# Kernel tuning notes

Hardware: AMD Instinct MI355X
Metric: run time of the kernel (lower is better)

Reference implementation:

```python
import jax, jax.numpy as jnp
import numpy as np

TOP_K = 2


def setup_inputs() -> dict:
    key = jax.random.key(0)
    k0, k1, k2, k3 = jax.random.split(key, 4)
    T, H, E, I = 512, 2048, 16, 1024  # tokens, hidden, experts, intermediate
    return {
        "hidden_states": jax.random.normal(k0, (T, H), jnp.float32),
        "router_weight": jax.random.normal(k1, (E, H), jnp.float32) * 0.02,
        "w13": jax.random.normal(k2, (E, H, 2 * I), jnp.float32) * 0.02,  # fused gate+up
        "w2": jax.random.normal(k3, (E, I, H), jnp.float32) * 0.02,        # down proj
    }


def reference(hidden_states, router_weight, w13, w2):
    x = hidden_states                                   # [T, H]
    E = router_weight.shape[0]
    # Router: linear (no bias) -> softmax -> top-k -> renormalize
    logits = x @ router_weight.T                        # [T, E]
    probs = jax.nn.softmax(logits, axis=-1)
    vals, idx = jax.lax.top_k(probs, TOP_K)             # [T, K]
    vals = vals / jnp.sum(vals, axis=-1, keepdims=True)
    # Dense combine weights [T, E]: zero except the top-k experts per token
    cw = jnp.sum(jax.nn.one_hot(idx, E, dtype=x.dtype) * vals[..., None], axis=1)
    # Scan over experts; each expert runs a SwiGLU MLP over all tokens,
    # scaled by its (mostly-zero) combine weight. Keeps peak memory at [T, I].
    def body(acc, params):
        w13_e, w2_e, cw_e = params                      # [H,2I], [I,H], [T]
        g, u = jnp.split(x @ w13_e, 2, axis=-1)         # [T, I] each
        acc = acc + cw_e[:, None] * ((jax.nn.silu(g) * u) @ w2_e)
        return acc, None
    out, _ = jax.lax.scan(body, jnp.zeros_like(x), (w13, w2, cw.T))
    return out
```

## Files before the change

kernel.cpp:

```cpp
#include <hip/hip_runtime.h>

#define T_TOK 512
#define HID   2048
#define NEXP  16
#define IDIM  1024
#define KC    64
#define WSTRIDE 2048

typedef __attribute__((ext_vector_type(8)))  short bf16x8;
typedef __attribute__((ext_vector_type(16))) float f32x16;
typedef __attribute__((ext_vector_type(4)))  float float4v;

__device__ __forceinline__ unsigned short f2bf(float f) {
    union { float f; unsigned u; } v; v.f = f;
    return (unsigned short)((v.u + 0x7FFFu + ((v.u >> 16) & 1u)) >> 16);
}

__device__ __forceinline__ bf16x8 pack8(const float* s) {
    bf16x8 r;
#pragma unroll
    for (int i = 0; i < 8; ++i) r[i] = (short)f2bf(s[i]);
    return r;
}

__global__ __launch_bounds__(256) void router_kernel(
    const float* __restrict__ x, const float* __restrict__ rw,
    int* __restrict__ cnt, int* __restrict__ tok,
    int* __restrict__ rowid, float* __restrict__ wt,
    unsigned short* __restrict__ xb)
{
    int t = blockIdx.x;
    int tid = threadIdx.x;
    const float* xr = x + (size_t)t * HID;

    {
        int c = tid * 8;
        float4v a = *(const float4v*)(xr + c);
        float4v b = *(const float4v*)(xr + c + 4);
        float tmp[8];
#pragma unroll
        for (int i = 0; i < 4; ++i) { tmp[i] = a[i]; tmp[4 + i] = b[i]; }
        *(bf16x8*)(xb + (size_t)t * HID + c) = pack8(tmp);
    }

    float acc[NEXP];
#pragma unroll
    for (int e = 0; e < NEXP; ++e) acc[e] = 0.f;

    for (int k = tid; k < HID; k += 256) {
        float xv = xr[k];
#pragma unroll
        for (int e = 0; e < NEXP; ++e) acc[e] += xv * rw[e * HID + k];
    }

    __shared__ float red[4][NEXP];
    int lane = tid & 63, wv = tid >> 6;
#pragma unroll
    for (int e = 0; e < NEXP; ++e) {
        float v = acc[e];
#pragma unroll
        for (int off = 32; off > 0; off >>= 1) v += __shfl_down(v, off);
        if (lane == 0) red[wv][e] = v;
    }
    __syncthreads();

    if (tid == 0) {
        float l[NEXP];
        float mx = -1e30f;
#pragma unroll
        for (int e = 0; e < NEXP; ++e) {
            l[e] = red[0][e] + red[1][e] + red[2][e] + red[3][e];
            mx = fmaxf(mx, l[e]);
        }
        float s = 0.f;
#pragma unroll
        for (int e = 0; e < NEXP; ++e) { l[e] = __expf(l[e] - mx); s += l[e]; }
        float inv_s = 1.f / s;
        int i0 = 0; float v0 = -1.f;
        int i1 = 0; float v1 = -2.f;
#pragma unroll
        for (int e = 0; e < NEXP; ++e) {
            float p = l[e] * inv_s;
            if (p > v0)      { v1 = v0; i1 = i0; v0 = p; i0 = e; }
            else if (p > v1) { v1 = p; i1 = e; }
        }
        float inv = 1.f / (v0 + v1);
        int p0 = atomicAdd(&cnt[i0], 1);
        tok[i0 * T_TOK + p0] = t; rowid[i0 * T_TOK + p0] = 2 * t;     wt[i0 * T_TOK + p0] = v0 * inv;
        int p1 = atomicAdd(&cnt[i1], 1);
        tok[i1 * T_TOK + p1] = t; rowid[i1 * T_TOK + p1] = 2 * t + 1; wt[i1 * T_TOK + p1] = v1 * inv;
    }
}

#define LOADW(r, kk_) { _Pragma("unroll") for (int j = 0; j < 8; ++j) \
    r[j] = wsrc[(size_t)((kk_) + kq * 8 + j) * WSTRIDE]; }

#define STOREW(r, bufi) { \
    *(bf16x8*)((char*)Ws[bufi] + ((wcol * 128 + kq * 16) ^ ((wcol & 7) << 4))) = pack8(r); }

#define LOADX(r, kk_) { \
    r[0] = *(const bf16x8*)(xsrc + (kk_)); \
    r[1] = *(const bf16x8*)(xsrc + (kk_) + 8); }

#define STOREX(r, bufi) { \
    *(bf16x8*)((char*)Xs[bufi] + ((xrow * 128 + xq * 32)      ^ xswz)) = r[0]; \
    *(bf16x8*)((char*)Xs[bufi] + ((xrow * 128 + xq * 32 + 16) ^ xswz)) = r[1]; }

__global__ __launch_bounds__(512, 4) void gemm1_kernel(
    const unsigned short* __restrict__ xb, const float* __restrict__ w13,
    const int* __restrict__ cnt, const int* __restrict__ tok,
    const int* __restrict__ rowid, const float* __restrict__ wt,
    unsigned short* __restrict__ h)
{
    int bid = blockIdx.x;
    int e   = bid >> 5;
    int c0h = (bid & 31) * 32;
    int n = cnt[e];
    int tid = threadIdx.x;

    __shared__ __align__(16) short Xs[2][128 * KC];
    __shared__ __align__(16) short Ws[2][64 * KC];
    __shared__ float Ex[4][16][64];
    __shared__ int   tks[128];
    __shared__ int   rws[128];
    __shared__ float wts[128];

    const float* wbase = w13 + (size_t)e * HID * (2 * IDIM);

    int wcol = tid & 63, kq = tid >> 6;
    const float* wsrc = wbase + ((wcol < 32) ? (c0h + wcol)
                                             : (IDIM + c0h + (wcol - 32)));
    int xrow = tid >> 2, xq = tid & 3;
    int xswz = (xrow & 7) << 4;

    int wave = tid >> 6, lane = tid & 63;
    int wm = wave & 3, wn = wave >> 2;
    int lrow = lane & 31, lhalf = lane >> 5;
    int swz = (lrow & 7) << 4;

#define G1_MFMA(bufi) { if (wm * 32 < nt) { _Pragma("unroll") \
    for (int s = 0; s < 4; ++s) { \
        int kb = s * 32 + lhalf * 16; \
        bf16x8 a = *(const bf16x8*)((char*)Xs[bufi] + (((wm * 32 + lrow) * 128 + kb) ^ swz)); \
        bf16x8 b = *(const bf16x8*)((char*)Ws[bufi] + (((wn * 32 + lrow) * 128 + kb) ^ swz)); \
        acc = __builtin_amdgcn_mfma_f32_32x32x16_bf16(a, b, acc, 0, 0, 0); \
    } } }

    for (int t0 = 0; t0 < n; t0 += 128) {
        int nt = min(128, n - t0);
        __syncthreads();
        if (tid < 128) {
            int idx = t0 + min(tid, nt - 1);
            tks[tid] = tok[e * T_TOK + idx];
            rws[tid] = rowid[e * T_TOK + idx];
            wts[tid] = wt[e * T_TOK + idx];
        }
        __syncthreads();

        const unsigned short* xsrc = xb + (size_t)tks[xrow] * HID + xq * 16;

        f32x16 acc = (f32x16)0.f;
        float  rWa[8], rWb[8];
        bf16x8 rXa[2], rXb[2];

        LOADW(rWa, 0);  LOADX(rXa, 0);
        LOADW(rWb, KC); LOADX(rXb, KC);
        STOREW(rWa, 0); STOREX(rXa, 0);
        __syncthreads();

        for (int p = 0; p < HID / KC; p += 2) {
            int kf0 = (p + 2) * KC, kf1 = (p + 3) * KC;
            if (kf0 < HID) { LOADW(rWa, kf0); LOADX(rXa, kf0); }
            G1_MFMA(0);
            STOREW(rWb, 1); STOREX(rXb, 1);
            __syncthreads();
            if (kf1 < HID) { LOADW(rWb, kf1); LOADX(rXb, kf1); }
            G1_MFMA(1);
            if (kf0 < HID) { STOREW(rWa, 0); STOREX(rXa, 0); }
            __syncthreads();
        }

        if (wn == 1) {
#pragma unroll
            for (int q = 0; q < 16; ++q) Ex[wm][q][lane] = acc[q];
        }
        __syncthreads();
        if (wn == 0) {
#pragma unroll
            for (int q = 0; q < 16; ++q) {
                int r = wm * 32 + (q & 3) + 8 * (q >> 2) + 4 * lhalf;
                if (r < nt) {
                    float g = acc[q];
                    float u = Ex[wm][q][lane];
                    float sg = g / (1.f + __expf(-g));
                    h[(size_t)rws[r] * IDIM + c0h + lrow] = f2bf(wts[r] * sg * u);
                }
            }
        }
    }
}

__global__ __launch_bounds__(512, 4) void gemm2_kernel(
    const unsigned short* __restrict__ h, const float* __restrict__ w2,
    const int* __restrict__ cnt, const int* __restrict__ tok,
    const int* __restrict__ rowid,
    float* __restrict__ out)
{
    int bid = blockIdx.x;
    int e  = bid >> 5;
    int c0 = (bid & 31) * 64;
    int n = cnt[e];
    int tid = threadIdx.x;

    __shared__ __align__(16) short Xs[2][128 * KC];
    __shared__ __align__(16) short Ws[2][64 * KC];
    __shared__ int   tks[128];
    __shared__ int   rws[128];

    const float* wbase = w2 + (size_t)e * IDIM * HID;

    int wcol = tid & 63, kq = tid >> 6;
    const float* wsrc = wbase + c0 + wcol;
    int xrow = tid >> 2, xq = tid & 3;
    int xswz = (xrow & 7) << 4;

    int wave = tid >> 6, lane = tid & 63;
    int wm = wave & 3, wn = wave >> 2;
    int lrow = lane & 31, lhalf = lane >> 5;
    int swz = (lrow & 7) << 4;

#define G2_MFMA(bufi) { if (wm * 32 < nt) { _Pragma("unroll") \
    for (int s = 0; s < 4; ++s) { \
        int kb = s * 32 + lhalf * 16; \
        bf16x8 a = *(const bf16x8*)((char*)Xs[bufi] + (((wm * 32 + lrow) * 128 + kb) ^ swz)); \
        bf16x8 b = *(const bf16x8*)((char*)Ws[bufi] + (((wn * 32 + lrow) * 128 + kb) ^ swz)); \
        acc = __builtin_amdgcn_mfma_f32_32x32x16_bf16(a, b, acc, 0, 0, 0); \
    } } }

    for (int t0 = 0; t0 < n; t0 += 128) {
        int nt = min(128, n - t0);
        __syncthreads();
        if (tid < 128) {
            int idx = t0 + min(tid, nt - 1);
            tks[tid] = tok[e * T_TOK + idx];
            rws[tid] = rowid[e * T_TOK + idx];
        }
        __syncthreads();

        const unsigned short* xsrc = h + (size_t)rws[xrow] * IDIM + xq * 16;

        f32x16 acc = (f32x16)0.f;
        float  rWa[8], rWb[8];
        bf16x8 rXa[2], rXb[2];

        LOADW(rWa, 0);  LOADX(rXa, 0);
        LOADW(rWb, KC); LOADX(rXb, KC);
        STOREW(rWa, 0); STOREX(rXa, 0);
        __syncthreads();

        for (int p = 0; p < IDIM / KC; p += 2) {
            int kf0 = (p + 2) * KC, kf1 = (p + 3) * KC;
            if (kf0 < IDIM) { LOADW(rWa, kf0); LOADX(rXa, kf0); }
            G2_MFMA(0);
            STOREW(rWb, 1); STOREX(rXb, 1);
            __syncthreads();
            if (kf1 < IDIM) { LOADW(rWb, kf1); LOADX(rXb, kf1); }
            G2_MFMA(1);
            if (kf0 < IDIM) { STOREW(rWa, 0); STOREX(rXa, 0); }
            __syncthreads();
        }

#pragma unroll
        for (int q = 0; q < 16; ++q) {
            int r = wm * 32 + (q & 3) + 8 * (q >> 2) + 4 * lhalf;
            if (r < nt)
                atomicAdd(&out[(size_t)tks[r] * HID + c0 + wn * 32 + lrow], acc[q]);
        }
    }
}

extern "C" void kernel_launch(void* const* d_in, const int* in_sizes, int n_in,
                              void* d_out, int out_size, void* d_ws, size_t ws_size,
                              hipStream_t stream) {
    const float* x   = (const float*)d_in[0];
    const float* rw  = (const float*)d_in[1];
    const float* w13 = (const float*)d_in[2];
    const float* w2  = (const float*)d_in[3];
    float* out = (float*)d_out;

    int* cnt   = (int*)d_ws;
    int* tok   = cnt + 64;
    int* rowid = tok + NEXP * T_TOK;
    float* wt  = (float*)(rowid + NEXP * T_TOK);
    unsigned short* h  = (unsigned short*)((char*)d_ws + 131072);
    unsigned short* xb = (unsigned short*)((char*)d_ws + 131072 + 2097152);

    hipMemsetAsync(out, 0, (size_t)T_TOK * HID * sizeof(float), stream);
    hipMemsetAsync(cnt, 0, 64 * sizeof(int), stream);

    router_kernel<<<T_TOK, 256, 0, stream>>>(x, rw, cnt, tok, rowid, wt, xb);
    gemm1_kernel<<<512, 512, 0, stream>>>(xb, w13, cnt, tok, rowid, wt, h);
    gemm2_kernel<<<512, 512, 0, stream>>>(h, w2, cnt, tok, rowid, out);
}
```

Baseline: 134.6 us.

## Split-K both expert GEMMs with wider tiles, atomic accumulation and separate SiLU pass

Both GEMMs are restructured as split-K. Each block now covers a 256-column by 512-row (gemm1) or 256-row (gemm2) K slice and uses 1024 threads with two accumulators per wave. Gemm1 atomically accumulates fp32 gate/up partials into a new workspace buffer, and a new silu_kernel applies SiLU, the gate×up product and the routing weight, storing bf16 h. This targets the long serial K loops and low per-block parallelism, and makes each block's weight loads wider. The cost is an extra memset and kernel launch, fp32 atomic traffic on the gate/up buffer, and loss of the double-buffered LDS pipeline.

```diff
diff --git a/kernel.cpp b/kernel.cpp
--- a/kernel.cpp
+++ b/kernel.cpp
@@ -5,7 +5,7 @@
 #define NEXP  16
 #define IDIM  1024
 #define KC    64
-#define WSTRIDE 2048
+#define W2I   2048
 
 typedef __attribute__((ext_vector_type(8)))  short bf16x8;
 typedef __attribute__((ext_vector_type(16))) float f32x16;
@@ -26,7 +26,7 @@
 __global__ __launch_bounds__(256) void router_kernel(
     const float* __restrict__ x, const float* __restrict__ rw,
     int* __restrict__ cnt, int* __restrict__ tok,
-    int* __restrict__ rowid, float* __restrict__ wt,
+    int* __restrict__ rowid, float* __restrict__ wtrow,
     unsigned short* __restrict__ xb)
 {
     int t = blockIdx.x;
@@ -86,65 +86,42 @@
         }
         float inv = 1.f / (v0 + v1);
         int p0 = atomicAdd(&cnt[i0], 1);
-        tok[i0 * T_TOK + p0] = t; rowid[i0 * T_TOK + p0] = 2 * t;     wt[i0 * T_TOK + p0] = v0 * inv;
+        tok[i0 * T_TOK + p0] = t; rowid[i0 * T_TOK + p0] = 2 * t;
         int p1 = atomicAdd(&cnt[i1], 1);
-        tok[i1 * T_TOK + p1] = t; rowid[i1 * T_TOK + p1] = 2 * t + 1; wt[i1 * T_TOK + p1] = v1 * inv;
-    }
-}
-
-#define LOADW(r, kk_) { _Pragma("unroll") for (int j = 0; j < 8; ++j) \
-    r[j] = wsrc[(size_t)((kk_) + kq * 8 + j) * WSTRIDE]; }
-
-#define STOREW(r, bufi) { \
-    *(bf16x8*)((char*)Ws[bufi] + ((wcol * 128 + kq * 16) ^ ((wcol & 7) << 4))) = pack8(r); }
-
-#define LOADX(r, kk_) { \
-    r[0] = *(const bf16x8*)(xsrc + (kk_)); \
-    r[1] = *(const bf16x8*)(xsrc + (kk_) + 8); }
-
-#define STOREX(r, bufi) { \
-    *(bf16x8*)((char*)Xs[bufi] + ((xrow * 128 + xq * 32)      ^ xswz)) = r[0]; \
-    *(bf16x8*)((char*)Xs[bufi] + ((xrow * 128 + xq * 32 + 16) ^ xswz)) = r[1]; }
-
-__global__ __launch_bounds__(512, 4) void gemm1_kernel(
+        tok[i1 * T_TOK + p1] = t; rowid[i1 * T_TOK + p1] = 2 * t + 1;
+        wtrow[2 * t]     = v0 * inv;
+        wtrow[2 * t + 1] = v1 * inv;
+    }
+}
+
+__global__ __launch_bounds__(1024, 4) void gemm1_kernel(
     const unsigned short* __restrict__ xb, const float* __restrict__ w13,
     const int* __restrict__ cnt, const int* __restrict__ tok,
-    const int* __restrict__ rowid, const float* __restrict__ wt,
-    unsigned short* __restrict__ h)
+    const int* __restrict__ rowid,
+    float* __restrict__ gu)
 {
     int bid = blockIdx.x;
     int e   = bid >> 5;
-    int c0h = (bid & 31) * 32;
+    int c0  = ((bid >> 2) & 7) * 256;
+    int kc0 = (bid & 3) * 512;
     int n = cnt[e];
     int tid = threadIdx.x;
 
-    __shared__ __align__(16) short Xs[2][128 * KC];
-    __shared__ __align__(16) short Ws[2][64 * KC];
-    __shared__ float Ex[4][16][64];
-    __shared__ int   tks[128];
-    __shared__ int   rws[128];
-    __shared__ float wts[128];
-
-    const float* wbase = w13 + (size_t)e * HID * (2 * IDIM);
-
-    int wcol = tid & 63, kq = tid >> 6;
-    const float* wsrc = wbase + ((wcol < 32) ? (c0h + wcol)
-                                             : (IDIM + c0h + (wcol - 32)));
-    int xrow = tid >> 2, xq = tid & 3;
+    __shared__ __align__(16) short Xs[128 * KC];
+    __shared__ __align__(16) short Ws[256 * KC];
+    __shared__ int tks[128];
+    __shared__ int rws[128];
+
+    int wcol = tid & 255, kq = (tid >> 8) & 3;
+    const float* wsrc = w13 + (size_t)e * HID * W2I + c0 + wcol;
+    int wswz = (wcol & 7) << 4;
+    int xrow = tid >> 3, xq = tid & 7;
     int xswz = (xrow & 7) << 4;
 
     int wave = tid >> 6, lane = tid & 63;
     int wm = wave & 3, wn = wave >> 2;
     int lrow = lane & 31, lhalf = lane >> 5;
     int swz = (lrow & 7) << 4;
-
-#define G1_MFMA(bufi) { if (wm * 32 < nt) { _Pragma("unroll") \
-    for (int s = 0; s < 4; ++s) { \
-        int kb = s * 32 + lhalf * 16; \
-        bf16x8 a = *(const bf16x8*)((char*)Xs[bufi] + (((wm * 32 + lrow) * 128 + kb) ^ swz)); \
-        bf16x8 b = *(const bf16x8*)((char*)Ws[bufi] + (((wn * 32 + lrow) * 128 + kb) ^ swz)); \
-        acc = __builtin_amdgcn_mfma_f32_32x32x16_bf16(a, b, acc, 0, 0, 0); \
-    } } }
 
     for (int t0 = 0; t0 < n; t0 += 128) {
         int nt = min(128, n - t0);
@@ -153,89 +130,106 @@
             int idx = t0 + min(tid, nt - 1);
             tks[tid] = tok[e * T_TOK + idx];
             rws[tid] = rowid[e * T_TOK + idx];
-            wts[tid] = wt[e * T_TOK + idx];
         }
         __syncthreads();
 
-        const unsigned short* xsrc = xb + (size_t)tks[xrow] * HID + xq * 16;
-
-        f32x16 acc = (f32x16)0.f;
-        float  rWa[8], rWb[8];
-        bf16x8 rXa[2], rXb[2];
-
-        LOADW(rWa, 0);  LOADX(rXa, 0);
-        LOADW(rWb, KC); LOADX(rXb, KC);
-        STOREW(rWa, 0); STOREX(rXa, 0);
-        __syncthreads();
-
-        for (int p = 0; p < HID / KC; p += 2) {
-            int kf0 = (p + 2) * KC, kf1 = (p + 3) * KC;
-            if (kf0 < HID) { LOADW(rWa, kf0); LOADX(rXa, kf0); }
-            G1_MFMA(0);
-            STOREW(rWb, 1); STOREX(rXb, 1);
+        const unsigned short* xsrc = xb + (size_t)tks[xrow] * HID + kc0 + xq * 8;
+
+        f32x16 acc0 = (f32x16)0.f, acc1 = (f32x16)0.f;
+        float  rW[16];
+        bf16x8 rX;
+
+#pragma unroll
+        for (int j = 0; j < 16; ++j)
+            rW[j] = wsrc[(size_t)(kc0 + kq * 16 + j) * W2I];
+        rX = *(const bf16x8*)(xsrc);
+
+        for (int p = 0; p < 8; ++p) {
+            *(bf16x8*)((char*)Ws + ((wcol * 128 + kq * 32)      ^ wswz)) = pack8(&rW[0]);
+            *(bf16x8*)((char*)Ws + ((wcol * 128 + kq * 32 + 16) ^ wswz)) = pack8(&rW[8]);
+            *(bf16x8*)((char*)Xs + ((xrow * 128 + xq * 16) ^ xswz)) = rX;
+            if (p < 7) {
+                int k0n = kc0 + (p + 1) * KC;
+#pragma unroll
+                for (int j = 0; j < 16; ++j)
+                    rW[j] = wsrc[(size_t)(k0n + kq * 16 + j) * W2I];
+                rX = *(const bf16x8*)(xsrc + (p + 1) * KC);
+            }
             __syncthreads();
-            if (kf1 < HID) { LOADW(rWb, kf1); LOADX(rXb, kf1); }
-            G1_MFMA(1);
-            if (kf0 < HID) { STOREW(rWa, 0); STOREX(rXa, 0); }
+            if (wm * 32 < nt) {
+#pragma unroll
+                for (int s = 0; s < 4; ++s) {
+                    int kb = s * 32 + lhalf * 16;
+                    bf16x8 a  = *(const bf16x8*)((char*)Xs + (((wm * 32 + lrow) * 128 + kb) ^ swz));
+                    bf16x8 b0 = *(const bf16x8*)((char*)Ws + (((wn * 64 + lrow) * 128 + kb) ^ swz));
+                    acc0 = __builtin_amdgcn_mfma_f32_32x32x16_bf16(a, b0, acc0, 0, 0, 0);
+                    bf16x8 b1 = *(const bf16x8*)((char*)Ws + (((wn * 64 + 32 + lrow) * 128 + kb) ^ swz));
+                    acc1 = __builtin_amdgcn_mfma_f32_32x32x16_bf16(a, b1, acc1, 0, 0, 0);
+                }
+            }
             __syncthreads();
         }
 
-        if (wn == 1) {
-#pragma unroll
-            for (int q = 0; q < 16; ++q) Ex[wm][q][lane] = acc[q];
-        }
-        __syncthreads();
-        if (wn == 0) {
-#pragma unroll
-            for (int q = 0; q < 16; ++q) {
-                int r = wm * 32 + (q & 3) + 8 * (q >> 2) + 4 * lhalf;
-                if (r < nt) {
-                    float g = acc[q];
-                    float u = Ex[wm][q][lane];
-                    float sg = g / (1.f + __expf(-g));
-                    h[(size_t)rws[r] * IDIM + c0h + lrow] = f2bf(wts[r] * sg * u);
-                }
-            }
-        }
-    }
-}
-
-__global__ __launch_bounds__(512, 4) void gemm2_kernel(
+#pragma unroll
+        for (int q = 0; q < 16; ++q) {
+            int r = wm * 32 + (q & 3) + 8 * (q >> 2) + 4 * lhalf;
+            if (r < nt) {
+                size_t rowb = (size_t)rws[r] * W2I + c0 + wn * 64 + lrow;
+                atomicAdd(&gu[rowb], acc0[q]);
+                atomicAdd(&gu[rowb + 32], acc1[q]);
+            }
+        }
+    }
+}
+
+__global__ __launch_bounds__(256) void silu_kernel(
+    const float* __restrict__ gu, const float* __restrict__ wtrow,
+    unsigned short* __restrict__ h)
+{
+    int r = blockIdx.x;
+    int c = threadIdx.x * 4;
+    float w = wtrow[r];
+    float4v g = *(const float4v*)(gu + (size_t)r * W2I + c);
+    float4v u = *(const float4v*)(gu + (size_t)r * W2I + IDIM + c);
+    unsigned o01, o23;
+    float s0 = g[0] / (1.f + __expf(-g[0])) * u[0] * w;
+    float s1 = g[1] / (1.f + __expf(-g[1])) * u[1] * w;
+    float s2 = g[2] / (1.f + __expf(-g[2])) * u[2] * w;
+    float s3 = g[3] / (1.f + __expf(-g[3])) * u[3] * w;
+    o01 = (unsigned)f2bf(s0) | ((unsigned)f2bf(s1) << 16);
+    o23 = (unsigned)f2bf(s2) | ((unsigned)f2bf(s3) << 16);
+    unsigned* dst = (unsigned*)(h + (size_t)r * IDIM + c);
+    dst[0] = o01; dst[1] = o23;
+}
+
+__global__ __launch_bounds__(1024, 4) void gemm2_kernel(
     const unsigned short* __restrict__ h, const float* __restrict__ w2,
     const int* __restrict__ cnt, const int* __restrict__ tok,
     const int* __restrict__ rowid,
     float* __restrict__ out)
 {
     int bid = blockIdx.x;
-    int e  = bid >> 5;
-    int c0 = (bid & 31) * 64;
+    int e   = bid >> 5;
+    int c0  = ((bid >> 2) & 7) * 256;
+    int kc0 = (bid & 3) * 256;
     int n = cnt[e];
     int tid = threadIdx.x;
 
-    __shared__ __align__(16) short Xs[2][128 * KC];
-    __shared__ __align__(16) short Ws[2][64 * KC];
-    __shared__ int   tks[128];
-    __shared__ int   rws[128];
-
-    const float* wbase = w2 + (size_t)e * IDIM * HID;
-
-    int wcol = tid & 63, kq = tid >> 6;
-    const float* wsrc = wbase + c0 + wcol;
-    int xrow = tid >> 2, xq = tid & 3;
+    __shared__ __align__(16) short Xs[128 * KC];
+    __shared__ __align__(16) short Ws[256 * KC];
+    __shared__ int tks[128];
+    __shared__ int rws[128];
+
+    int wcol = tid & 255, kq = (tid >> 8) & 3;
+    const float* wsrc = w2 + (size_t)e * IDIM * HID + c0 + wcol;
+    int wswz = (wcol & 7) << 4;
+    int xrow = tid >> 3, xq = tid & 7;
     int xswz = (xrow & 7) << 4;
 
     int wave = tid >> 6, lane = tid & 63;
     int wm = wave & 3, wn = wave >> 2;
     int lrow = lane & 31, lhalf = lane >> 5;
     int swz = (lrow & 7) << 4;
-
-#define G2_MFMA(bufi) { if (wm * 32 < nt) { _Pragma("unroll") \
-    for (int s = 0; s < 4; ++s) { \
-        int kb = s * 32 + lhalf * 16; \
-        bf16x8 a = *(const bf16x8*)((char*)Xs[bufi] + (((wm * 32 + lrow) * 128 + kb) ^ swz)); \
-        bf16x8 b = *(const bf16x8*)((char*)Ws[bufi] + (((wn * 32 + lrow) * 128 + kb) ^ swz)); \
-        acc = __builtin_amdgcn_mfma_f32_32x32x16_bf16(a, b, acc, 0, 0, 0); \
-    } } }
 
     for (int t0 = 0; t0 < n; t0 += 128) {
         int nt = min(128, n - t0);
@@ -247,34 +241,51 @@
         }
         __syncthreads();
 
-        const unsigned short* xsrc = h + (size_t)rws[xrow] * IDIM + xq * 16;
-
-        f32x16 acc = (f32x16)0.f;
-        float  rWa[8], rWb[8];
-        bf16x8 rXa[2], rXb[2];
-
-        LOADW(rWa, 0);  LOADX(rXa, 0);
-        LOADW(rWb, KC); LOADX(rXb, KC);
-        STOREW(rWa, 0); STOREX(rXa, 0);
-        __syncthreads();
-
-        for (int p = 0; p < IDIM / KC; p += 2) {
-            int kf0 = (p + 2) * KC, kf1 = (p + 3) * KC;
-            if (kf0 < IDIM) { LOADW(rWa, kf0); LOADX(rXa, kf0); }
-            G2_MFMA(0);
-            STOREW(rWb, 1); STOREX(rXb, 1);
+        const unsigned short* xsrc = h + (size_t)rws[xrow] * IDIM + kc0 + xq * 8;
+
+        f32x16 acc0 = (f32x16)0.f, acc1 = (f32x16)0.f;
+        float  rW[16];
+        bf16x8 rX;
+
+#pragma unroll
+        for (int j = 0; j < 16; ++j)
+            rW[j] = wsrc[(size_t)(kc0 + kq * 16 + j) * W2I];
+        rX = *(const bf16x8*)(xsrc);
+
+        for (int p = 0; p < 4; ++p) {
+            *(bf16x8*)((char*)Ws + ((wcol * 128 + kq * 32)      ^ wswz)) = pack8(&rW[0]);
+            *(bf16x8*)((char*)Ws + ((wcol * 128 + kq * 32 + 16) ^ wswz)) = pack8(&rW[8]);
+            *(bf16x8*)((char*)Xs + ((xrow * 128 + xq * 16) ^ xswz)) = rX;
+            if (p < 3) {
+                int k0n = kc0 + (p + 1) * KC;
+#pragma unroll
+                for (int j = 0; j < 16; ++j)
+                    rW[j] = wsrc[(size_t)(k0n + kq * 16 + j) * W2I];
+                rX = *(const bf16x8*)(xsrc + (p + 1) * KC);
+            }
             __syncthreads();
-            if (kf1 < IDIM) { LOADW(rWb, kf1); LOADX(rXb, kf1); }
-            G2_MFMA(1);
-            if (kf0 < IDIM) { STOREW(rWa, 0); STOREX(rXa, 0); }
+            if (wm * 32 < nt) {
+#pragma unroll
+                for (int s = 0; s < 4; ++s) {
+                    int kb = s * 32 + lhalf * 16;
+                    bf16x8 a  = *(const bf16x8*)((char*)Xs + (((wm * 32 + lrow) * 128 + kb) ^ swz));
+                    bf16x8 b0 = *(const bf16x8*)((char*)Ws + (((wn * 64 + lrow) * 128 + kb) ^ swz));
+                    acc0 = __builtin_amdgcn_mfma_f32_32x32x16_bf16(a, b0, acc0, 0, 0, 0);
+                    bf16x8 b1 = *(const bf16x8*)((char*)Ws + (((wn * 64 + 32 + lrow) * 128 + kb) ^ swz));
+                    acc1 = __builtin_amdgcn_mfma_f32_32x32x16_bf16(a, b1, acc1, 0, 0, 0);
+                }
+            }
             __syncthreads();
         }
 
 #pragma unroll
         for (int q = 0; q < 16; ++q) {
             int r = wm * 32 + (q & 3) + 8 * (q >> 2) + 4 * lhalf;
-            if (r < nt)
-                atomicAdd(&out[(size_t)tks[r] * HID + c0 + wn * 32 + lrow], acc[q]);
+            if (r < nt) {
+                size_t ob = (size_t)tks[r] * HID + c0 + wn * 64 + lrow;
+                atomicAdd(&out[ob], acc0[q]);
+                atomicAdd(&out[ob + 32], acc1[q]);
+            }
         }
     }
 }
@@ -288,17 +299,21 @@
     const float* w2  = (const float*)d_in[3];
     float* out = (float*)d_out;
 
-    int* cnt   = (int*)d_ws;
-    int* tok   = cnt + 64;
-    int* rowid = tok + NEXP * T_TOK;
-    float* wt  = (float*)(rowid + NEXP * T_TOK);
-    unsigned short* h  = (unsigned short*)((char*)d_ws + 131072);
-    unsigned short* xb = (unsigned short*)((char*)d_ws + 131072 + 2097152);
+    char* ws = (char*)d_ws;
+    int*   cnt   = (int*)ws;
+    int*   tok   = (int*)(ws + 1024);
+    int*   rowid = (int*)(ws + 1024 + 32768);
+    float* wtrow = (float*)(ws + 1024 + 65536);
+    unsigned short* h  = (unsigned short*)(ws + 131072);
+    unsigned short* xb = (unsigned short*)(ws + 131072 + 2097152);
+    float* gu = (float*)(ws + 131072 + 2 * 2097152);
 
     hipMemsetAsync(out, 0, (size_t)T_TOK * HID * sizeof(float), stream);
-    hipMemsetAsync(cnt, 0, 64 * sizeof(int), stream);
-
-    router_kernel<<<T_TOK, 256, 0, stream>>>(x, rw, cnt, tok, rowid, wt, xb);
-    gemm1_kernel<<<512, 512, 0, stream>>>(xb, w13, cnt, tok, rowid, wt, h);
-    gemm2_kernel<<<512, 512, 0, stream>>>(h, w2, cnt, tok, rowid, out);
-}
+    hipMemsetAsync(cnt, 0, 1024, stream);
+    hipMemsetAsync(gu, 0, (size_t)1024 * W2I * sizeof(float), stream);
+
+    router_kernel<<<T_TOK, 256, 0, stream>>>(x, rw, cnt, tok, rowid, wtrow, xb);
+    gemm1_kernel<<<512, 1024, 0, stream>>>(xb, w13, cnt, tok, rowid, gu);
+    silu_kernel<<<1024, 256, 0, stream>>>(gu, wtrow, h);
+    gemm2_kernel<<<512, 1024, 0, stream>>>(h, w2, cnt, tok, rowid, out);
+}
```

After: 164.3 us. +22.1%, slower.

## Stage large token chunks in LDS and stream fp32 weights directly into MFMA registers

Applied to the files above, without the earlier changes.

Both expert GEMM kernels are restructured. Each block now stages a 128x512 bf16 token slice in a 128KB shared buffer, and each wave loads its weight B-fragments straight from global memory into registers, packing them to bf16 without a shared-memory round trip. Each wave computes two 32x32 output tiles, reusing one B fragment across two MFMAs, and the grid is halved to 256 blocks with larger column tiles. This removes the weight LDS staging and its per-step barriers, at the cost of lower occupancy, uncoalesced strided weight loads per lane, and fewer blocks to fill the GPU.

```diff
diff --git a/kernel.cpp b/kernel.cpp
--- a/kernel.cpp
+++ b/kernel.cpp
@@ -4,8 +4,6 @@
 #define HID   2048
 #define NEXP  16
 #define IDIM  1024
-#define KC    64
-#define WSTRIDE 2048
 
 typedef __attribute__((ext_vector_type(8)))  short bf16x8;
 typedef __attribute__((ext_vector_type(16))) float f32x16;
@@ -92,59 +90,46 @@
     }
 }
 
-#define LOADW(r, kk_) { _Pragma("unroll") for (int j = 0; j < 8; ++j) \
-    r[j] = wsrc[(size_t)((kk_) + kq * 8 + j) * WSTRIDE]; }
-
-#define STOREW(r, bufi) { \
-    *(bf16x8*)((char*)Ws[bufi] + ((wcol * 128 + kq * 16) ^ ((wcol & 7) << 4))) = pack8(r); }
-
-#define LOADX(r, kk_) { \
-    r[0] = *(const bf16x8*)(xsrc + (kk_)); \
-    r[1] = *(const bf16x8*)(xsrc + (kk_) + 8); }
-
-#define STOREX(r, bufi) { \
-    *(bf16x8*)((char*)Xs[bufi] + ((xrow * 128 + xq * 32)      ^ xswz)) = r[0]; \
-    *(bf16x8*)((char*)Xs[bufi] + ((xrow * 128 + xq * 32 + 16) ^ xswz)) = r[1]; }
-
-__global__ __launch_bounds__(512, 4) void gemm1_kernel(
+#define STAGE_X(SRCROW) { \
+    const bf16x8* src16 = (const bf16x8*)((SRCROW) + kc0 + xseg * 128); \
+    _Pragma("unroll") \
+    for (int q = 0; q < 16; ++q) { \
+        bf16x8 v = src16[q]; \
+        *(bf16x8*)((char*)Xs + ((xrow * 1024 + xseg * 256 + q * 16) ^ xswz)) = v; \
+    } }
+
+#define LOADB(buf, p_) { _Pragma("unroll") \
+    for (int j = 0; j < 8; ++j) \
+        buf[j] = wsrc[(size_t)(kc0 + (p_) * 16 + j) * 2048]; }
+
+__global__ __launch_bounds__(512, 2) void gemm1_kernel(
     const unsigned short* __restrict__ xb, const float* __restrict__ w13,
     const int* __restrict__ cnt, const int* __restrict__ tok,
     const int* __restrict__ rowid, const float* __restrict__ wt,
     unsigned short* __restrict__ h)
 {
     int bid = blockIdx.x;
-    int e   = bid >> 5;
-    int c0h = (bid & 31) * 32;
+    int e    = bid >> 4;
+    int tile = bid & 15;
     int n = cnt[e];
     int tid = threadIdx.x;
 
-    __shared__ __align__(16) short Xs[2][128 * KC];
-    __shared__ __align__(16) short Ws[2][64 * KC];
-    __shared__ float Ex[4][16][64];
+    __shared__ __align__(16) short Xs[65536];
     __shared__ int   tks[128];
     __shared__ int   rws[128];
     __shared__ float wts[128];
 
-    const float* wbase = w13 + (size_t)e * HID * (2 * IDIM);
-
-    int wcol = tid & 63, kq = tid >> 6;
-    const float* wsrc = wbase + ((wcol < 32) ? (c0h + wcol)
-                                             : (IDIM + c0h + (wcol - 32)));
-    int xrow = tid >> 2, xq = tid & 3;
+    int xrow = tid >> 2, xseg = tid & 3;
     int xswz = (xrow & 7) << 4;
 
     int wave = tid >> 6, lane = tid & 63;
-    int wm = wave & 3, wn = wave >> 2;
-    int lrow = lane & 31, lhalf = lane >> 5;
+    int wm = wave & 1, wn = wave >> 1;
+    int lrow = lane & 31, hi = lane >> 5;
     int swz = (lrow & 7) << 4;
 
-#define G1_MFMA(bufi) { if (wm * 32 < nt) { _Pragma("unroll") \
-    for (int s = 0; s < 4; ++s) { \
-        int kb = s * 32 + lhalf * 16; \
-        bf16x8 a = *(const bf16x8*)((char*)Xs[bufi] + (((wm * 32 + lrow) * 128 + kb) ^ swz)); \
-        bf16x8 b = *(const bf16x8*)((char*)Ws[bufi] + (((wn * 32 + lrow) * 128 + kb) ^ swz)); \
-        acc = __builtin_amdgcn_mfma_f32_32x32x16_bf16(a, b, acc, 0, 0, 0); \
-    } } }
+    int col = (wn < 2) ? (tile * 64 + wn * 32 + lrow)
+                       : (IDIM + tile * 64 + (wn - 2) * 32 + lrow);
+    const float* wsrc = w13 + (size_t)e * HID * 2048 + col + (size_t)hi * 8 * 2048;
 
     for (int t0 = 0; t0 < n; t0 += 128) {
         int nt = min(128, n - t0);
@@ -157,85 +142,105 @@
         }
         __syncthreads();
 
-        const unsigned short* xsrc = xb + (size_t)tks[xrow] * HID + xq * 16;
-
-        f32x16 acc = (f32x16)0.f;
-        float  rWa[8], rWb[8];
-        bf16x8 rXa[2], rXb[2];
-
-        LOADW(rWa, 0);  LOADX(rXa, 0);
-        LOADW(rWb, KC); LOADX(rXb, KC);
-        STOREW(rWa, 0); STOREX(rXa, 0);
-        __syncthreads();
-
-        for (int p = 0; p < HID / KC; p += 2) {
-            int kf0 = (p + 2) * KC, kf1 = (p + 3) * KC;
-            if (kf0 < HID) { LOADW(rWa, kf0); LOADX(rXa, kf0); }
-            G1_MFMA(0);
-            STOREW(rWb, 1); STOREX(rXb, 1);
+        const unsigned short* xrowp = xb + (size_t)tks[xrow] * HID;
+        bool g0 = (wm * 64) < nt, g1 = (wm * 64 + 32) < nt;
+        int r0 = (wm * 64 + lrow) * 1024;
+        int r1 = r0 + 32 * 1024;
+
+        f32x16 acc0 = (f32x16)0.f, acc1 = (f32x16)0.f;
+
+        for (int c = 0; c < 4; ++c) {
+            int kc0 = c * 512;
+            STAGE_X(xrowp);
             __syncthreads();
-            if (kf1 < HID) { LOADW(rWb, kf1); LOADX(rXb, kf1); }
-            G1_MFMA(1);
-            if (kf0 < HID) { STOREW(rWa, 0); STOREX(rXa, 0); }
+
+            float b0[8], b1[8];
+            LOADB(b0, 0); LOADB(b1, 1);
+#pragma unroll 4
+            for (int p = 0; p < 32; p += 2) {
+                bf16x8 bfr = pack8(b0);
+                if (p + 2 < 32) LOADB(b0, p + 2);
+                {
+                    int kb = p * 32 + hi * 16;
+                    bf16x8 a0 = *(const bf16x8*)((char*)Xs + ((r0 + kb) ^ swz));
+                    bf16x8 a1 = *(const bf16x8*)((char*)Xs + ((r1 + kb) ^ swz));
+                    if (g0) acc0 = __builtin_amdgcn_mfma_f32_32x32x16_bf16(a0, bfr, acc0, 0, 0, 0);
+                    if (g1) acc1 = __builtin_amdgcn_mfma_f32_32x32x16_bf16(a1, bfr, acc1, 0, 0, 0);
+                }
+                bf16x8 bfr1 = pack8(b1);
+                if (p + 3 < 32) LOADB(b1, p + 3);
+                {
+                    int kb = (p + 1) * 32 + hi * 16;
+                    bf16x8 a0 = *(const bf16x8*)((char*)Xs + ((r0 + kb) ^ swz));
+                    bf16x8 a1 = *(const bf16x8*)((char*)Xs + ((r1 + kb) ^ swz));
+                    if (g0) acc0 = __builtin_amdgcn_mfma_f32_32x32x16_bf16(a0, bfr1, acc0, 0, 0, 0);
+                    if (g1) acc1 = __builtin_amdgcn_mfma_f32_32x32x16_bf16(a1, bfr1, acc1, 0, 0, 0);
+                }
+                if ((p & 7) == 6) __builtin_amdgcn_s_barrier();
+            }
             __syncthreads();
         }
 
-        if (wn == 1) {
-#pragma unroll
-            for (int q = 0; q < 16; ++q) Ex[wm][q][lane] = acc[q];
-        }
-        __syncthreads();
-        if (wn == 0) {
+        float* Ex = (float*)Xs;
+        if (wn >= 2) {
+            int base = ((wm * 2 + (wn - 2)) * 2) * 1024;
 #pragma unroll
             for (int q = 0; q < 16; ++q) {
-                int r = wm * 32 + (q & 3) + 8 * (q >> 2) + 4 * lhalf;
-                if (r < nt) {
-                    float g = acc[q];
-                    float u = Ex[wm][q][lane];
+                Ex[base + q * 64 + lane] = acc0[q];
+                Ex[base + 1024 + q * 64 + lane] = acc1[q];
+            }
+        }
+        __syncthreads();
+        if (wn < 2) {
+            int base = ((wm * 2 + wn) * 2) * 1024;
+            int hcol = tile * 64 + wn * 32 + lrow;
+#pragma unroll
+            for (int q = 0; q < 16; ++q) {
+                int crow = (q & 3) + 8 * (q >> 2) + 4 * hi;
+                int ra = wm * 64 + crow;
+                if (ra < nt) {
+                    float g = acc0[q], u = Ex[base + q * 64 + lane];
                     float sg = g / (1.f + __expf(-g));
-                    h[(size_t)rws[r] * IDIM + c0h + lrow] = f2bf(wts[r] * sg * u);
+                    h[(size_t)rws[ra] * IDIM + hcol] = f2bf(wts[ra] * sg * u);
+                }
+                int rb = wm * 64 + 32 + crow;
+                if (rb < nt) {
+                    float g = acc1[q], u = Ex[base + 1024 + q * 64 + lane];
+                    float sg = g / (1.f + __expf(-g));
+                    h[(size_t)rws[rb] * IDIM + hcol] = f2bf(wts[rb] * sg * u);
                 }
             }
         }
-    }
-}
-
-__global__ __launch_bounds__(512, 4) void gemm2_kernel(
+        __syncthreads();
+    }
+}
+
+__global__ __launch_bounds__(512, 2) void gemm2_kernel(
     const unsigned short* __restrict__ h, const float* __restrict__ w2,
     const int* __restrict__ cnt, const int* __restrict__ tok,
     const int* __restrict__ rowid,
     float* __restrict__ out)
 {
     int bid = blockIdx.x;
-    int e  = bid >> 5;
-    int c0 = (bid & 31) * 64;
+    int e    = bid >> 4;
+    int tile = bid & 15;
     int n = cnt[e];
     int tid = threadIdx.x;
 
-    __shared__ __align__(16) short Xs[2][128 * KC];
-    __shared__ __align__(16) short Ws[2][64 * KC];
-    __shared__ int   tks[128];
-    __shared__ int   rws[128];
-
-    const float* wbase = w2 + (size_t)e * IDIM * HID;
-
-    int wcol = tid & 63, kq = tid >> 6;
-    const float* wsrc = wbase + c0 + wcol;
-    int xrow = tid >> 2, xq = tid & 3;
+    __shared__ __align__(16) short Xs[65536];
+    __shared__ int tks[128];
+    __shared__ int rws[128];
+
+    int xrow = tid >> 2, xseg = tid & 3;
     int xswz = (xrow & 7) << 4;
 
     int wave = tid >> 6, lane = tid & 63;
-    int wm = wave & 3, wn = wave >> 2;
-    int lrow = lane & 31, lhalf = lane >> 5;
+    int wm = wave & 1, wn = wave >> 1;
+    int lrow = lane & 31, hi = lane >> 5;
     int swz = (lrow & 7) << 4;
 
-#define G2_MFMA(bufi) { if (wm * 32 < nt) { _Pragma("unroll") \
-    for (int s = 0; s < 4; ++s) { \
-        int kb = s * 32 + lhalf * 16; \
-        bf16x8 a = *(const bf16x8*)((char*)Xs[bufi] + (((wm * 32 + lrow) * 128 + kb) ^ swz)); \
-        bf16x8 b = *(const bf16x8*)((char*)Ws[bufi] + (((wn * 32 + lrow) * 128 + kb) ^ swz)); \
-        acc = __builtin_amdgcn_mfma_f32_32x32x16_bf16(a, b, acc, 0, 0, 0); \
-    } } }
+    int col = tile * 128 + wn * 32 + lrow;
+    const float* wsrc = w2 + (size_t)e * IDIM * 2048 + col + (size_t)hi * 8 * 2048;
 
     for (int t0 = 0; t0 < n; t0 += 128) {
         int nt = min(128, n - t0);
@@ -247,35 +252,54 @@
         }
         __syncthreads();
 
-        const unsigned short* xsrc = h + (size_t)rws[xrow] * IDIM + xq * 16;
-
-        f32x16 acc = (f32x16)0.f;
-        float  rWa[8], rWb[8];
-        bf16x8 rXa[2], rXb[2];
-
-        LOADW(rWa, 0);  LOADX(rXa, 0);
-        LOADW(rWb, KC); LOADX(rXb, KC);
-        STOREW(rWa, 0); STOREX(rXa, 0);
-        __syncthreads();
-
-        for (int p = 0; p < IDIM / KC; p += 2) {
-            int kf0 = (p + 2) * KC, kf1 = (p + 3) * KC;
-            if (kf0 < IDIM) { LOADW(rWa, kf0); LOADX(rXa, kf0); }
-            G2_MFMA(0);
-            STOREW(rWb, 1); STOREX(rXb, 1);
+        const unsigned short* xrowp = h + (size_t)rws[xrow] * IDIM;
+        bool g0 = (wm * 64) < nt, g1 = (wm * 64 + 32) < nt;
+        int r0 = (wm * 64 + lrow) * 1024;
+        int r1 = r0 + 32 * 1024;
+
+        f32x16 acc0 = (f32x16)0.f, acc1 = (f32x16)0.f;
+
+        for (int c = 0; c < 2; ++c) {
+            int kc0 = c * 512;
+            STAGE_X(xrowp);
             __syncthreads();
-            if (kf1 < IDIM) { LOADW(rWb, kf1); LOADX(rXb, kf1); }
-            G2_MFMA(1);
-            if (kf0 < IDIM) { STOREW(rWa, 0); STOREX(rXa, 0); }
+
+            float b0[8], b1[8];
+            LOADB(b0, 0); LOADB(b1, 1);
+#pragma unroll 4
+            for (int p = 0; p < 32; p += 2) {
+                bf16x8 bfr = pack8(b0);
+                if (p + 2 < 32) LOADB(b0, p + 2);
+                {
+                    int kb = p * 32 + hi * 16;
+                    bf16x8 a0 = *(const bf16x8*)((char*)Xs + ((r0 + kb) ^ swz));
+                    bf16x8 a1 = *(const bf16x8*)((char*)Xs + ((r1 + kb) ^ swz));
+                    if (g0) acc0 = __builtin_amdgcn_mfma_f32_32x32x16_bf16(a0, bfr, acc0, 0, 0, 0);
+                    if (g1) acc1 = __builtin_amdgcn_mfma_f32_32x32x16_bf16(a1, bfr, acc1, 0, 0, 0);
+                }
+                bf16x8 bfr1 = pack8(b1);
+                if (p + 3 < 32) LOADB(b1, p + 3);
+                {
+                    int kb = (p + 1) * 32 + hi * 16;
+                    bf16x8 a0 = *(const bf16x8*)((char*)Xs + ((r0 + kb) ^ swz));
+                    bf16x8 a1 = *(const bf16x8*)((char*)Xs + ((r1 + kb) ^ swz));
+                    if (g0) acc0 = __builtin_amdgcn_mfma_f32_32x32x16_bf16(a0, bfr1, acc0, 0, 0, 0);
+                    if (g1) acc1 = __builtin_amdgcn_mfma_f32_32x32x16_bf16(a1, bfr1, acc1, 0, 0, 0);
+                }
+                if ((p & 7) == 6) __builtin_amdgcn_s_barrier();
+            }
             __syncthreads();
         }
 
 #pragma unroll
         for (int q = 0; q < 16; ++q) {
-            int r = wm * 32 + (q & 3) + 8 * (q >> 2) + 4 * lhalf;
-            if (r < nt)
-                atomicAdd(&out[(size_t)tks[r] * HID + c0 + wn * 32 + lrow], acc[q]);
-        }
+            int crow = (q & 3) + 8 * (q >> 2) + 4 * hi;
+            int ra = wm * 64 + crow;
+            if (ra < nt) atomicAdd(&out[(size_t)tks[ra] * HID + col], acc0[q]);
+            int rb = wm * 64 + 32 + crow;
+            if (rb < nt) atomicAdd(&out[(size_t)tks[rb] * HID + col], acc1[q]);
+        }
+        __syncthreads();
     }
 }
 
@@ -288,17 +312,18 @@
     const float* w2  = (const float*)d_in[3];
     float* out = (float*)d_out;
 
-    int* cnt   = (int*)d_ws;
-    int* tok   = cnt + 64;
-    int* rowid = tok + NEXP * T_TOK;
-    float* wt  = (float*)(rowid + NEXP * T_TOK);
-    unsigned short* h  = (unsigned short*)((char*)d_ws + 131072);
-    unsigned short* xb = (unsigned short*)((char*)d_ws + 131072 + 2097152);
+    char* ws = (char*)d_ws;
+    int*   cnt   = (int*)ws;
+    int*   tok   = (int*)(ws + 1024);
+    int*   rowid = (int*)(ws + 1024 + 32768);
+    float* wt    = (float*)(ws + 1024 + 65536);
+    unsigned short* h  = (unsigned short*)(ws + 131072);
+    unsigned short* xb = (unsigned short*)(ws + 131072 + 2097152);
 
     hipMemsetAsync(out, 0, (size_t)T_TOK * HID * sizeof(float), stream);
-    hipMemsetAsync(cnt, 0, 64 * sizeof(int), stream);
+    hipMemsetAsync(cnt, 0, 1024, stream);
 
     router_kernel<<<T_TOK, 256, 0, stream>>>(x, rw, cnt, tok, rowid, wt, xb);
-    gemm1_kernel<<<512, 512, 0, stream>>>(xb, w13, cnt, tok, rowid, wt, h);
-    gemm2_kernel<<<512, 512, 0, stream>>>(h, w2, cnt, tok, rowid, out);
-}
+    gemm1_kernel<<<256, 512, 0, stream>>>(xb, w13, cnt, tok, rowid, wt, h);
+    gemm2_kernel<<<256, 512, 0, stream>>>(h, w2, cnt, tok, rowid, out);
+}
```

New measurement: 146.1 us. 1.09x slower.
